# Optimization experiments

Hardware: AMD Instinct MI355X
Metric: run time of the kernel (lower is better)

The kernel has to match this reference:

```python
import jax, jax.numpy as jnp
import numpy as np

N_NODES = 100000
N_EDGES = 1600000
D_IN = 128
D_OUT = 128
EPS = 1e-12  # F.normalize default eps


def setup_inputs() -> dict:
    key = jax.random.key(0)
    k1, k2, k3, k4, k5 = jax.random.split(key, 5)
    x = jax.random.normal(k1, (N_NODES, D_IN), dtype=jnp.float32)
    edge_index = jax.random.randint(k2, (2, N_EDGES), 0, N_NODES, dtype=jnp.int64)
    # PyG SAGEConv params: lin_l (neighbor path, with bias), lin_r (root path, no bias)
    s = 1.0 / np.sqrt(D_IN)
    W_l = jax.random.uniform(k3, (D_IN, D_OUT), jnp.float32, -s, s)
    b_l = jax.random.uniform(k4, (D_OUT,), jnp.float32, -s, s)
    W_r = jax.random.uniform(k5, (D_IN, D_OUT), jnp.float32, -s, s)
    return {"x": x, "edge_index": edge_index, "W_l": W_l, "b_l": b_l, "W_r": W_r}


def reference(x, edge_index, W_l, b_l, W_r):
    n = x.shape[0]
    src = edge_index[0]  # message source nodes (x_j)
    dst = edge_index[1]  # aggregation targets (i)
    # gather + mean scatter-reduce
    msg = x[src]                                            # [E, D_IN]
    summed = jax.ops.segment_sum(msg, dst, num_segments=n)  # [N, D_IN]
    cnt = jax.ops.segment_sum(jnp.ones((msg.shape[0],), x.dtype), dst, num_segments=n)
    mean = summed / jnp.maximum(cnt, 1.0)[:, None]
    # lin_l(mean) + lin_r(x), then row-wise L2 normalize
    out = mean @ W_l + b_l + x @ W_r                        # [N, D_OUT]
    norm = jnp.sqrt(jnp.sum(out * out, axis=-1, keepdims=True))
    return out / jnp.maximum(norm, EPS)
```

## Files before the change

kernel.cpp:

```cpp
#include <hip/hip_runtime.h>
#include <hip/hip_bf16.h>

#define N_NODES 100000
#define N_EDGES 1600000
#define D 128
#define TILES (N_NODES / 16)
#define WPB 8
#define NB2 782
#define NPB2 128
#define CAP 4096
#define EPB 8192
#define PBLK 196

typedef __attribute__((ext_vector_type(4))) float f32x4;
typedef __attribute__((ext_vector_type(8))) short short8;
typedef __attribute__((ext_vector_type(4))) unsigned int u32x4;
typedef __attribute__((ext_vector_type(2))) unsigned int u32x2;

static __device__ __forceinline__ unsigned short f2bf(float f) {
  unsigned u = __float_as_uint(f);
  u += 0x7fffu + ((u >> 16) & 1u);
  return (unsigned short)(u >> 16);
}

static __device__ __forceinline__ void acc4(u32x2 u, float& a0, float& a1,
                                            float& a2, float& a3) {
  a0 += __uint_as_float(u[0] << 16);
  a1 += __uint_as_float(u[0] & 0xffff0000u);
  a2 += __uint_as_float(u[1] << 16);
  a3 += __uint_as_float(u[1] & 0xffff0000u);
}

__global__ __launch_bounds__(256) void prepw_k(const float* __restrict__ Wl,
                                               const float* __restrict__ Wr,
                                               unsigned short* __restrict__ wt_g) {
  int i = blockIdx.x * 256 + threadIdx.x;
  int k = i >> 7, c = i & 127;
  float w = (k < 128) ? Wl[k * 128 + c] : Wr[(k - 128) * 128 + c];
  int phys = (k >> 3) ^ (c & 7);
  wt_g[c * 256 + (phys << 3) + (k & 7)] = f2bf(w);
}

__global__ __launch_bounds__(256) void cvt_k(const float* __restrict__ x,
                                             unsigned* __restrict__ xh) {
  size_t i = (size_t)blockIdx.x * 256 + threadIdx.x;
  const f32x4* p = (const f32x4*)(x + i * 8);
  f32x4 v0 = p[0], v1 = p[1];
  u32x4 o;
  o[0] = ((unsigned)f2bf(v0[1]) << 16) | f2bf(v0[0]);
  o[1] = ((unsigned)f2bf(v0[3]) << 16) | f2bf(v0[2]);
  o[2] = ((unsigned)f2bf(v1[1]) << 16) | f2bf(v1[0]);
  o[3] = ((unsigned)f2bf(v1[3]) << 16) | f2bf(v1[2]);
  *(u32x4*)(xh + i * 4) = o;
}

__global__ __launch_bounds__(256) void p3b_k(const int* __restrict__ ei,
                                             int* __restrict__ btail,
                                             unsigned* __restrict__ part) {
  __shared__ int bh[NB2], lbase[NB2], lcur[NB2];
  int t = threadIdx.x;
  for (int i = t; i < NB2; i += 256) { bh[i] = 0; lcur[i] = 0; }
  __syncthreads();
  int base = blockIdx.x * EPB;
  int end = min(base + EPB, N_EDGES);
  for (int i = base + t; i < end; i += 256)
    atomicAdd(&bh[ei[N_EDGES + i] >> 7], 1);
  __syncthreads();
  for (int i = t; i < NB2; i += 256)
    if (bh[i]) lbase[i] = atomicAdd(&btail[i], bh[i]);
  __syncthreads();
  for (int i = base + t; i < end; i += 256) {
    int dst = ei[N_EDGES + i];
    int src = ei[i];
    int b = dst >> 7;
    int pos = lbase[b] + atomicAdd(&lcur[b], 1);
    if (pos < CAP)
      part[(size_t)b * CAP + pos] =
          ((unsigned)(dst & (NPB2 - 1)) << 17) | (unsigned)src;
  }
}

__global__ __launch_bounds__(512) void g3_k(const unsigned* __restrict__ xh,
                                            const unsigned* __restrict__ part,
                                            const int* __restrict__ btail,
                                            unsigned* __restrict__ mh) {
  __shared__ int s_deg[NPB2], s_ptr[NPB2], s_off[NPB2];
  __shared__ int s_csr[CAP];
  int t = threadIdx.x, b = blockIdx.x;
  int ne = min(btail[b], CAP);
  if (t < NPB2) s_deg[t] = 0;
  __syncthreads();
  const unsigned* pp = part + (size_t)b * CAP;
  for (int i = t; i < ne; i += 512) atomicAdd(&s_deg[pp[i] >> 17], 1);
  __syncthreads();
  if (t < NPB2) s_ptr[t] = s_deg[t];
  __syncthreads();
  for (int o = 1; o < NPB2; o <<= 1) {
    int u = (t >= o && t < NPB2) ? s_ptr[t - o] : 0;
    __syncthreads();
    if (t < NPB2) s_ptr[t] += u;
    __syncthreads();
  }
  if (t < NPB2) {
    int ex = s_ptr[t] - s_deg[t];
    s_ptr[t] = ex;
    s_off[t] = ex;
  }
  __syncthreads();
  for (int i = t; i < ne; i += 512) {
    unsigned c = pp[i];
    int pos = atomicAdd(&s_off[c >> 17], 1);
    s_csr[pos] = (int)(c & 0x1FFFFu);
  }
  __syncthreads();

  int wv = t >> 6, lane = t & 63, half = lane >> 5, lh = lane & 31;
  for (int p = 0; p < 8; p++) {
    int nl = (wv * 8 + p) * 2 + half;
    int node = b * NPB2 + nl;
    bool valid = node < N_NODES;
    int deg = valid ? s_deg[nl] : 0;
    int bse = valid ? s_ptr[nl] : 0;
    float a0 = 0.f, a1 = 0.f, a2 = 0.f, a3 = 0.f;
    float b0 = 0.f, b1 = 0.f, b2 = 0.f, b3 = 0.f;
    for (int c = 0; c < deg; c += 32) {
      int rem = deg - c;
      int n = min(32, rem);
      int eidx = (lh < rem) ? s_csr[bse + c + lh] : 0;
      int j = 0;
      for (; j + 7 < n; j += 8) {
        int s0 = __shfl(eidx, j, 32);
        int s1 = __shfl(eidx, j + 1, 32);
        int s2 = __shfl(eidx, j + 2, 32);
        int s3 = __shfl(eidx, j + 3, 32);
        int s4 = __shfl(eidx, j + 4, 32);
        int s5 = __shfl(eidx, j + 5, 32);
        int s6 = __shfl(eidx, j + 6, 32);
        int s7 = __shfl(eidx, j + 7, 32);
        u32x2 u0 = *(const u32x2*)(xh + (size_t)s0 * 64 + lh * 2);
        u32x2 u1 = *(const u32x2*)(xh + (size_t)s1 * 64 + lh * 2);
        u32x2 u2 = *(const u32x2*)(xh + (size_t)s2 * 64 + lh * 2);
        u32x2 u3 = *(const u32x2*)(xh + (size_t)s3 * 64 + lh * 2);
        u32x2 u4 = *(const u32x2*)(xh + (size_t)s4 * 64 + lh * 2);
        u32x2 u5 = *(const u32x2*)(xh + (size_t)s5 * 64 + lh * 2);
        u32x2 u6 = *(const u32x2*)(xh + (size_t)s6 * 64 + lh * 2);
        u32x2 u7 = *(const u32x2*)(xh + (size_t)s7 * 64 + lh * 2);
        acc4(u0, a0, a1, a2, a3);
        acc4(u1, b0, b1, b2, b3);
        acc4(u2, a0, a1, a2, a3);
        acc4(u3, b0, b1, b2, b3);
        acc4(u4, a0, a1, a2, a3);
        acc4(u5, b0, b1, b2, b3);
        acc4(u6, a0, a1, a2, a3);
        acc4(u7, b0, b1, b2, b3);
      }
      for (; j + 3 < n; j += 4) {
        int s0 = __shfl(eidx, j, 32);
        int s1 = __shfl(eidx, j + 1, 32);
        int s2 = __shfl(eidx, j + 2, 32);
        int s3 = __shfl(eidx, j + 3, 32);
        u32x2 u0 = *(const u32x2*)(xh + (size_t)s0 * 64 + lh * 2);
        u32x2 u1 = *(const u32x2*)(xh + (size_t)s1 * 64 + lh * 2);
        u32x2 u2 = *(const u32x2*)(xh + (size_t)s2 * 64 + lh * 2);
        u32x2 u3 = *(const u32x2*)(xh + (size_t)s3 * 64 + lh * 2);
        acc4(u0, a0, a1, a2, a3);
        acc4(u1, b0, b1, b2, b3);
        acc4(u2, a0, a1, a2, a3);
        acc4(u3, b0, b1, b2, b3);
      }
      for (; j < n; j++) {
        int s0 = __shfl(eidx, j, 32);
        u32x2 u0 = *(const u32x2*)(xh + (size_t)s0 * 64 + lh * 2);
        acc4(u0, a0, a1, a2, a3);
      }
    }
    if (valid) {
      float inv = 1.0f / fmaxf((float)deg, 1.0f);
      a0 = (a0 + b0) * inv;
      a1 = (a1 + b1) * inv;
      a2 = (a2 + b2) * inv;
      a3 = (a3 + b3) * inv;
      u32x2 o;
      o[0] = ((unsigned)f2bf(a1) << 16) | f2bf(a0);
      o[1] = ((unsigned)f2bf(a3) << 16) | f2bf(a2);
      *(u32x2*)(mh + (size_t)node * 64 + lh * 2) = o;
    }
  }
}

__global__ __launch_bounds__(512) void fused_k(
    const unsigned* __restrict__ xh, const unsigned* __restrict__ mh,
    const unsigned* __restrict__ wt_g, const float* __restrict__ bl,
    float* __restrict__ out) {
  __shared__ unsigned Wt[16384];

  int tid = threadIdx.x;
  {
    const u32x4* src = (const u32x4*)wt_g;
    u32x4* dst = (u32x4*)Wt;
    #pragma unroll
    for (int it = 0; it < 8; it++) dst[it * 512 + tid] = src[it * 512 + tid];
  }
  __syncthreads();

  int tile = blockIdx.x * WPB + (tid >> 6);
  if (tile >= TILES) return;
  int lane = tid & 63;
  int c0 = lane & 15;
  int g = lane >> 4;
  int row0 = tile * 16;
  const unsigned short* Wt16 = (const unsigned short*)Wt;

  f32x4 acc[8];
  #pragma unroll
  for (int ct = 0; ct < 8; ct++)
    for (int j = 0; j < 4; j++) acc[ct][j] = 0.0f;

  #pragma unroll
  for (int kf = 0; kf < 8; kf++) {
    int koff = (kf & 3) * 32 + g * 8;
    const unsigned short* a_src = (const unsigned short*)((kf < 4) ? mh : xh);
    short8 af = *(const short8*)(a_src + (size_t)(row0 + c0) * D + koff);
    #pragma unroll
    for (int ct = 0; ct < 8; ct++) {
      int c = ct * 16 + c0;
      short8 bf = *(const short8*)&Wt16[c * 256 + ((((kf << 2) + g) ^ (c & 7)) << 3)];
      acc[ct] = __builtin_amdgcn_mfma_f32_16x16x32_bf16(af, bf, acc[ct], 0, 0, 0);
    }
  }

  float ss[4] = {0.f, 0.f, 0.f, 0.f};
  #pragma unroll
  for (int ct = 0; ct < 8; ct++) {
    float bias = bl[ct * 16 + c0];
    #pragma unroll
    for (int j = 0; j < 4; j++) {
      float v = acc[ct][j] + bias;
      acc[ct][j] = v;
      ss[j] += v * v;
    }
  }
  #pragma unroll
  for (int j = 0; j < 4; j++) {
    float s = ss[j];
    s += __shfl_xor(s, 1);
    s += __shfl_xor(s, 2);
    s += __shfl_xor(s, 4);
    s += __shfl_xor(s, 8);
    ss[j] = 1.0f / fmaxf(sqrtf(s), 1e-12f);
  }
  #pragma unroll
  for (int ct = 0; ct < 8; ct++) {
    #pragma unroll
    for (int j = 0; j < 4; j++) {
      out[(size_t)(row0 + g * 4 + j) * D + ct * 16 + c0] = acc[ct][j] * ss[j];
    }
  }
}

extern "C" void kernel_launch(void* const* d_in, const int* in_sizes, int n_in,
                              void* d_out, int out_size, void* d_ws, size_t ws_size,
                              hipStream_t stream) {
  const float* x  = (const float*)d_in[0];
  const int*   ei = (const int*)d_in[1];
  const float* Wl = (const float*)d_in[2];
  const float* bl = (const float*)d_in[3];
  const float* Wr = (const float*)d_in[4];
  float* out = (float*)d_out;

  int* w = (int*)d_ws;
  int* btail = w;
  unsigned* part = (unsigned*)(w + 800);
  unsigned short* wt_g = (unsigned short*)(w + 3203872);
  const size_t XH_OFF = 3220256ULL * 4;
  const size_t MH_OFF = XH_OFF + (size_t)N_NODES * D * 2;
  unsigned* xh = (unsigned*)((char*)d_ws + XH_OFF);
  unsigned* mh = (unsigned*)((char*)d_ws + MH_OFF);

  hipMemsetAsync(btail, 0, 800 * sizeof(int), stream);
  prepw_k<<<128, 256, 0, stream>>>(Wl, Wr, wt_g);
  cvt_k<<<6250, 256, 0, stream>>>(x, xh);
  p3b_k<<<PBLK, 256, 0, stream>>>(ei, btail, part);
  g3_k<<<NB2, 512, 0, stream>>>(xh, part, btail, mh);
  fused_k<<<(TILES + WPB - 1) / WPB, 512, 0, stream>>>(xh, mh, (const unsigned*)wt_g, bl, out);
}
```

Baseline: 147.7 us.

## Merge preprocessing kernels and split bucket CSR build from gather

The weight prep, x-to-bf16 conversion and edge partitioning kernels are merged into one launch, with the block index choosing the role. The old g3 kernel is split in two. A CSR-building kernel sorts each bucket in place in global memory and writes per-node (offset, degree) pairs. A separate gather kernel with 12500 small blocks then does the neighbor mean. This removes launch gaps, lets the independent prep work run concurrently, and replaces the shared-memory-heavy 782-block gather with a finer grid for better occupancy and load balance. The cost is one extra global round-trip of the CSR indices.

```diff
diff --git a/kernel.cpp b/kernel.cpp
--- a/kernel.cpp
+++ b/kernel.cpp
@@ -11,6 +11,8 @@
 #define CAP 4096
 #define EPB 8192
 #define PBLK 196
+#define CVTB 6250
+#define PREPB 128
 
 typedef __attribute__((ext_vector_type(4))) float f32x4;
 typedef __attribute__((ext_vector_type(8))) short short8;
@@ -31,37 +33,36 @@
   a3 += __uint_as_float(u[1] & 0xffff0000u);
 }
 
-__global__ __launch_bounds__(256) void prepw_k(const float* __restrict__ Wl,
-                                               const float* __restrict__ Wr,
-                                               unsigned short* __restrict__ wt_g) {
-  int i = blockIdx.x * 256 + threadIdx.x;
-  int k = i >> 7, c = i & 127;
-  float w = (k < 128) ? Wl[k * 128 + c] : Wr[(k - 128) * 128 + c];
-  int phys = (k >> 3) ^ (c & 7);
-  wt_g[c * 256 + (phys << 3) + (k & 7)] = f2bf(w);
-}
-
-__global__ __launch_bounds__(256) void cvt_k(const float* __restrict__ x,
-                                             unsigned* __restrict__ xh) {
-  size_t i = (size_t)blockIdx.x * 256 + threadIdx.x;
-  const f32x4* p = (const f32x4*)(x + i * 8);
-  f32x4 v0 = p[0], v1 = p[1];
-  u32x4 o;
-  o[0] = ((unsigned)f2bf(v0[1]) << 16) | f2bf(v0[0]);
-  o[1] = ((unsigned)f2bf(v0[3]) << 16) | f2bf(v0[2]);
-  o[2] = ((unsigned)f2bf(v1[1]) << 16) | f2bf(v1[0]);
-  o[3] = ((unsigned)f2bf(v1[3]) << 16) | f2bf(v1[2]);
-  *(u32x4*)(xh + i * 4) = o;
-}
-
-__global__ __launch_bounds__(256) void p3b_k(const int* __restrict__ ei,
-                                             int* __restrict__ btail,
-                                             unsigned* __restrict__ part) {
+__global__ __launch_bounds__(256) void fuseA_k(
+    const float* __restrict__ x, unsigned* __restrict__ xh,
+    const int* __restrict__ ei, int* __restrict__ btail,
+    unsigned* __restrict__ part, const float* __restrict__ Wl,
+    const float* __restrict__ Wr, unsigned short* __restrict__ wt_g) {
   __shared__ int bh[NB2], lbase[NB2], lcur[NB2];
   int t = threadIdx.x;
+  if (blockIdx.x < CVTB) {
+    size_t i = (size_t)blockIdx.x * 256 + t;
+    const f32x4* p = (const f32x4*)(x + i * 8);
+    f32x4 v0 = p[0], v1 = p[1];
+    u32x4 o;
+    o[0] = ((unsigned)f2bf(v0[1]) << 16) | f2bf(v0[0]);
+    o[1] = ((unsigned)f2bf(v0[3]) << 16) | f2bf(v0[2]);
+    o[2] = ((unsigned)f2bf(v1[1]) << 16) | f2bf(v1[0]);
+    o[3] = ((unsigned)f2bf(v1[3]) << 16) | f2bf(v1[2]);
+    *(u32x4*)(xh + i * 4) = o;
+    return;
+  }
+  if (blockIdx.x >= CVTB + PBLK) {
+    int i = (blockIdx.x - CVTB - PBLK) * 256 + t;
+    int k = i >> 7, c = i & 127;
+    float w = (k < 128) ? Wl[k * 128 + c] : Wr[(k - 128) * 128 + c];
+    int phys = (k >> 3) ^ (c & 7);
+    wt_g[c * 256 + (phys << 3) + (k & 7)] = f2bf(w);
+    return;
+  }
   for (int i = t; i < NB2; i += 256) { bh[i] = 0; lcur[i] = 0; }
   __syncthreads();
-  int base = blockIdx.x * EPB;
+  int base = (blockIdx.x - CVTB) * EPB;
   int end = min(base + EPB, N_EDGES);
   for (int i = base + t; i < end; i += 256)
     atomicAdd(&bh[ei[N_EDGES + i] >> 7], 1);
@@ -80,112 +81,121 @@
   }
 }
 
-__global__ __launch_bounds__(512) void g3_k(const unsigned* __restrict__ xh,
-                                            const unsigned* __restrict__ part,
-                                            const int* __restrict__ btail,
-                                            unsigned* __restrict__ mh) {
-  __shared__ int s_deg[NPB2], s_ptr[NPB2], s_off[NPB2];
-  __shared__ int s_csr[CAP];
+__global__ __launch_bounds__(512) void p4c_k(unsigned* __restrict__ part,
+                                             const int* __restrict__ btail,
+                                             int2* __restrict__ pd) {
+  __shared__ unsigned s_codes[CAP];
+  __shared__ int s_deg[NPB2], s_scan[NPB2], s_off[NPB2];
   int t = threadIdx.x, b = blockIdx.x;
   int ne = min(btail[b], CAP);
+  unsigned* pp = part + (size_t)b * CAP;
+  for (int i = t; i < ne; i += 512) s_codes[i] = pp[i];
   if (t < NPB2) s_deg[t] = 0;
   __syncthreads();
-  const unsigned* pp = part + (size_t)b * CAP;
-  for (int i = t; i < ne; i += 512) atomicAdd(&s_deg[pp[i] >> 17], 1);
-  __syncthreads();
-  if (t < NPB2) s_ptr[t] = s_deg[t];
+  for (int i = t; i < ne; i += 512) atomicAdd(&s_deg[s_codes[i] >> 17], 1);
+  __syncthreads();
+  if (t < NPB2) s_scan[t] = s_deg[t];
   __syncthreads();
   for (int o = 1; o < NPB2; o <<= 1) {
-    int u = (t >= o && t < NPB2) ? s_ptr[t - o] : 0;
+    int u = (t >= o && t < NPB2) ? s_scan[t - o] : 0;
     __syncthreads();
-    if (t < NPB2) s_ptr[t] += u;
+    if (t < NPB2) s_scan[t] += u;
     __syncthreads();
   }
   if (t < NPB2) {
-    int ex = s_ptr[t] - s_deg[t];
-    s_ptr[t] = ex;
+    int deg = s_deg[t];
+    int ex = s_scan[t] - deg;
     s_off[t] = ex;
+    int node = b * NPB2 + t;
+    if (node < N_NODES) {
+      int2 v;
+      v.x = b * CAP + ex;
+      v.y = deg;
+      pd[node] = v;
+    }
   }
   __syncthreads();
   for (int i = t; i < ne; i += 512) {
-    unsigned c = pp[i];
+    unsigned c = s_codes[i];
     int pos = atomicAdd(&s_off[c >> 17], 1);
-    s_csr[pos] = (int)(c & 0x1FFFFu);
-  }
-  __syncthreads();
-
-  int wv = t >> 6, lane = t & 63, half = lane >> 5, lh = lane & 31;
-  for (int p = 0; p < 8; p++) {
-    int nl = (wv * 8 + p) * 2 + half;
-    int node = b * NPB2 + nl;
-    bool valid = node < N_NODES;
-    int deg = valid ? s_deg[nl] : 0;
-    int bse = valid ? s_ptr[nl] : 0;
-    float a0 = 0.f, a1 = 0.f, a2 = 0.f, a3 = 0.f;
-    float b0 = 0.f, b1 = 0.f, b2 = 0.f, b3 = 0.f;
-    for (int c = 0; c < deg; c += 32) {
-      int rem = deg - c;
-      int n = min(32, rem);
-      int eidx = (lh < rem) ? s_csr[bse + c + lh] : 0;
-      int j = 0;
-      for (; j + 7 < n; j += 8) {
-        int s0 = __shfl(eidx, j, 32);
-        int s1 = __shfl(eidx, j + 1, 32);
-        int s2 = __shfl(eidx, j + 2, 32);
-        int s3 = __shfl(eidx, j + 3, 32);
-        int s4 = __shfl(eidx, j + 4, 32);
-        int s5 = __shfl(eidx, j + 5, 32);
-        int s6 = __shfl(eidx, j + 6, 32);
-        int s7 = __shfl(eidx, j + 7, 32);
-        u32x2 u0 = *(const u32x2*)(xh + (size_t)s0 * 64 + lh * 2);
-        u32x2 u1 = *(const u32x2*)(xh + (size_t)s1 * 64 + lh * 2);
-        u32x2 u2 = *(const u32x2*)(xh + (size_t)s2 * 64 + lh * 2);
-        u32x2 u3 = *(const u32x2*)(xh + (size_t)s3 * 64 + lh * 2);
-        u32x2 u4 = *(const u32x2*)(xh + (size_t)s4 * 64 + lh * 2);
-        u32x2 u5 = *(const u32x2*)(xh + (size_t)s5 * 64 + lh * 2);
-        u32x2 u6 = *(const u32x2*)(xh + (size_t)s6 * 64 + lh * 2);
-        u32x2 u7 = *(const u32x2*)(xh + (size_t)s7 * 64 + lh * 2);
-        acc4(u0, a0, a1, a2, a3);
-        acc4(u1, b0, b1, b2, b3);
-        acc4(u2, a0, a1, a2, a3);
-        acc4(u3, b0, b1, b2, b3);
-        acc4(u4, a0, a1, a2, a3);
-        acc4(u5, b0, b1, b2, b3);
-        acc4(u6, a0, a1, a2, a3);
-        acc4(u7, b0, b1, b2, b3);
-      }
-      for (; j + 3 < n; j += 4) {
-        int s0 = __shfl(eidx, j, 32);
-        int s1 = __shfl(eidx, j + 1, 32);
-        int s2 = __shfl(eidx, j + 2, 32);
-        int s3 = __shfl(eidx, j + 3, 32);
-        u32x2 u0 = *(const u32x2*)(xh + (size_t)s0 * 64 + lh * 2);
-        u32x2 u1 = *(const u32x2*)(xh + (size_t)s1 * 64 + lh * 2);
-        u32x2 u2 = *(const u32x2*)(xh + (size_t)s2 * 64 + lh * 2);
-        u32x2 u3 = *(const u32x2*)(xh + (size_t)s3 * 64 + lh * 2);
-        acc4(u0, a0, a1, a2, a3);
-        acc4(u1, b0, b1, b2, b3);
-        acc4(u2, a0, a1, a2, a3);
-        acc4(u3, b0, b1, b2, b3);
-      }
-      for (; j < n; j++) {
-        int s0 = __shfl(eidx, j, 32);
-        u32x2 u0 = *(const u32x2*)(xh + (size_t)s0 * 64 + lh * 2);
-        acc4(u0, a0, a1, a2, a3);
-      }
-    }
-    if (valid) {
-      float inv = 1.0f / fmaxf((float)deg, 1.0f);
-      a0 = (a0 + b0) * inv;
-      a1 = (a1 + b1) * inv;
-      a2 = (a2 + b2) * inv;
-      a3 = (a3 + b3) * inv;
-      u32x2 o;
-      o[0] = ((unsigned)f2bf(a1) << 16) | f2bf(a0);
-      o[1] = ((unsigned)f2bf(a3) << 16) | f2bf(a2);
-      *(u32x2*)(mh + (size_t)node * 64 + lh * 2) = o;
-    }
-  }
+    pp[pos] = c & 0x1FFFFu;
+  }
+}
+
+__global__ __launch_bounds__(256) void gather2_k(const unsigned* __restrict__ xh,
+                                                 const unsigned* __restrict__ csr,
+                                                 const int2* __restrict__ pd,
+                                                 unsigned* __restrict__ mh) {
+  int wid = (blockIdx.x * 256 + threadIdx.x) >> 6;
+  int lane = threadIdx.x & 63;
+  int half = lane >> 5, lh = lane & 31;
+  int node = wid * 2 + half;
+  if (node >= N_NODES) return;
+  int2 v = pd[node];
+  int base = v.x;
+  int deg = v.y;
+  float a0 = 0.f, a1 = 0.f, a2 = 0.f, a3 = 0.f;
+  float b0 = 0.f, b1 = 0.f, b2 = 0.f, b3 = 0.f;
+  for (int c = 0; c < deg; c += 32) {
+    int rem = deg - c;
+    int n = min(32, rem);
+    int eidx = (lh < rem) ? (int)csr[base + c + lh] : 0;
+    int j = 0;
+    for (; j + 7 < n; j += 8) {
+      int s0 = __shfl(eidx, j, 32);
+      int s1 = __shfl(eidx, j + 1, 32);
+      int s2 = __shfl(eidx, j + 2, 32);
+      int s3 = __shfl(eidx, j + 3, 32);
+      int s4 = __shfl(eidx, j + 4, 32);
+      int s5 = __shfl(eidx, j + 5, 32);
+      int s6 = __shfl(eidx, j + 6, 32);
+      int s7 = __shfl(eidx, j + 7, 32);
+      u32x2 u0 = *(const u32x2*)(xh + (size_t)s0 * 64 + lh * 2);
+      u32x2 u1 = *(const u32x2*)(xh + (size_t)s1 * 64 + lh * 2);
+      u32x2 u2 = *(const u32x2*)(xh + (size_t)s2 * 64 + lh * 2);
+      u32x2 u3 = *(const u32x2*)(xh + (size_t)s3 * 64 + lh * 2);
+      u32x2 u4 = *(const u32x2*)(xh + (size_t)s4 * 64 + lh * 2);
+      u32x2 u5 = *(const u32x2*)(xh + (size_t)s5 * 64 + lh * 2);
+      u32x2 u6 = *(const u32x2*)(xh + (size_t)s6 * 64 + lh * 2);
+      u32x2 u7 = *(const u32x2*)(xh + (size_t)s7 * 64 + lh * 2);
+      acc4(u0, a0, a1, a2, a3);
+      acc4(u1, b0, b1, b2, b3);
+      acc4(u2, a0, a1, a2, a3);
+      acc4(u3, b0, b1, b2, b3);
+      acc4(u4, a0, a1, a2, a3);
+      acc4(u5, b0, b1, b2, b3);
+      acc4(u6, a0, a1, a2, a3);
+      acc4(u7, b0, b1, b2, b3);
+    }
+    for (; j + 3 < n; j += 4) {
+      int s0 = __shfl(eidx, j, 32);
+      int s1 = __shfl(eidx, j + 1, 32);
+      int s2 = __shfl(eidx, j + 2, 32);
+      int s3 = __shfl(eidx, j + 3, 32);
+      u32x2 u0 = *(const u32x2*)(xh + (size_t)s0 * 64 + lh * 2);
+      u32x2 u1 = *(const u32x2*)(xh + (size_t)s1 * 64 + lh * 2);
+      u32x2 u2 = *(const u32x2*)(xh + (size_t)s2 * 64 + lh * 2);
+      u32x2 u3 = *(const u32x2*)(xh + (size_t)s3 * 64 + lh * 2);
+      acc4(u0, a0, a1, a2, a3);
+      acc4(u1, b0, b1, b2, b3);
+      acc4(u2, a0, a1, a2, a3);
+      acc4(u3, b0, b1, b2, b3);
+    }
+    for (; j < n; j++) {
+      int s0 = __shfl(eidx, j, 32);
+      u32x2 u0 = *(const u32x2*)(xh + (size_t)s0 * 64 + lh * 2);
+      acc4(u0, a0, a1, a2, a3);
+    }
+  }
+  float inv = 1.0f / fmaxf((float)deg, 1.0f);
+  a0 = (a0 + b0) * inv;
+  a1 = (a1 + b1) * inv;
+  a2 = (a2 + b2) * inv;
+  a3 = (a3 + b3) * inv;
+  u32x2 o;
+  o[0] = ((unsigned)f2bf(a1) << 16) | f2bf(a0);
+  o[1] = ((unsigned)f2bf(a3) << 16) | f2bf(a2);
+  *(u32x2*)(mh + (size_t)node * 64 + lh * 2) = o;
 }
 
 __global__ __launch_bounds__(512) void fused_k(
@@ -270,17 +280,18 @@
 
   int* w = (int*)d_ws;
   int* btail = w;
-  unsigned* part = (unsigned*)(w + 800);
-  unsigned short* wt_g = (unsigned short*)(w + 3203872);
-  const size_t XH_OFF = 3220256ULL * 4;
+  int2* pd = (int2*)(w + 800);
+  unsigned* part = (unsigned*)(w + 200800);
+  unsigned short* wt_g = (unsigned short*)(w + 3403872);
+  const size_t XH_OFF = 3420256ULL * 4;
   const size_t MH_OFF = XH_OFF + (size_t)N_NODES * D * 2;
   unsigned* xh = (unsigned*)((char*)d_ws + XH_OFF);
   unsigned* mh = (unsigned*)((char*)d_ws + MH_OFF);
 
   hipMemsetAsync(btail, 0, 800 * sizeof(int), stream);
-  prepw_k<<<128, 256, 0, stream>>>(Wl, Wr, wt_g);
-  cvt_k<<<6250, 256, 0, stream>>>(x, xh);
-  p3b_k<<<PBLK, 256, 0, stream>>>(ei, btail, part);
-  g3_k<<<NB2, 512, 0, stream>>>(xh, part, btail, mh);
+  fuseA_k<<<CVTB + PBLK + PREPB, 256, 0, stream>>>(x, xh, ei, btail, part,
+                                                   Wl, Wr, wt_g);
+  p4c_k<<<NB2, 512, 0, stream>>>(part, btail, pd);
+  gather2_k<<<12500, 256, 0, stream>>>(xh, part, pd, mh);
   fused_k<<<(TILES + WPB - 1) / WPB, 512, 0, stream>>>(xh, mh, (const unsigned*)wt_g, bl, out);
 }
```

After: 152.6 us. 3.3% more time.
